# Kernel tuning notes

Measured on AMD Instinct MI355X. Metric: run time of the kernel, lower is better.

## Reference

```python
import jax, jax.numpy as jnp
import numpy as np

# dims: B batch, R seq_num (MSA rows), L seq_len (residues), D emb_dim, C n_emb_2D, H heads
B, R, L, D, C, H = 1, 256, 384, 512, 256, 4
HD = D // H
SCALE = np.float32((HD ** -0.5) / np.sqrt(L))  # head-dim scaling * seqlen_scaling (1/sqrt(L))
EPS = 1e-5


def setup_inputs() -> dict:
    key = jax.random.key(0)
    ks = jax.random.split(key, 6)
    s = 0.02
    return {
        "x": jax.random.normal(ks[0], (B, R, L, D), jnp.float32),
        "pair_feat": jax.random.normal(ks[1], (B, L, L, C), jnp.float32),
        "attn_mask": jnp.ones((B, L), jnp.int32),
        "ln_msa_g": jnp.ones((D,), jnp.float32),
        "ln_msa_b": jnp.zeros((D,), jnp.float32),
        "ln_pair_g": jnp.ones((C,), jnp.float32),
        "ln_pair_b": jnp.zeros((C,), jnp.float32),
        "W_pair": jax.random.normal(ks[2], (C, H), jnp.float32) * s,  # stacked per-head [C,1] linears
        "W_v": jax.random.normal(ks[3], (D, D), jnp.float32) * s,     # stacked per-head [D,HD] value proj
        "W_out": jax.random.normal(ks[4], (D, D), jnp.float32) * s,   # to_out (bias=False)
    }


def _ln(x, g, b):
    mu = jnp.mean(x, axis=-1, keepdims=True)
    var = jnp.mean(jnp.square(x - mu), axis=-1, keepdims=True)
    return (x - mu) * jax.lax.rsqrt(var + EPS) * g + b


def reference(x, pair_feat, attn_mask, ln_msa_g, ln_msa_b, ln_pair_g, ln_pair_b, W_pair, W_v, W_out):
    # MHPair_to_MSA.forward (eval mode, dropout=0)
    msa = _ln(x, ln_msa_g, ln_msa_b)                                  # [B,R,L,D]
    pf = (pair_feat + jnp.swapaxes(pair_feat, 1, 2)) * 0.5            # symmetrize
    pf = _ln(pf, ln_pair_g, ln_pair_b)                                # [B,L,L,C]
    # pair-feature-derived attention logits (no QK^T)
    logits = jnp.einsum('bijc,ch->bhij', pf * SCALE, W_pair)          # [B,H,L,L]
    V = jnp.einsum('brld,de->brle', msa, W_v).reshape(B, R, L, H, HD) # [B,R,L,H,HD]
    mask2 = attn_mask[:, :, None] * attn_mask[:, None, :]             # [B,L,L]
    logits = jnp.where(mask2[:, None, :, :] == 0,
                       jnp.finfo(logits.dtype).min, logits)
    attn = jax.nn.softmax(logits, axis=-1)                            # [B,H,L,L]
    out = jnp.einsum('bhij,brjhd->brihd', attn, V).reshape(B, R, L, D)
    out = out @ W_out                                                 # to_out, bias=False
    return x + out                                                    # residual
```

## Files before the change

### kernel.cpp

```cpp
#include <hip/hip_runtime.h>

#define L_   384
#define D_   512
#define C_   256
#define H_   4
#define RR_  256
#define M1_  98304
#define LL2_ 147456
#define NPAIR_BLOCKS 18480
#define TILE_ELEMS (128 * 64)
#define TILE256_ELEMS (256 * 64)

typedef __bf16 bf16x8 __attribute__((ext_vector_type(8)));
typedef float f32x4 __attribute__((ext_vector_type(4)));

__device__ __forceinline__ unsigned short f2bf_bits(float f) {
  union { float f; unsigned u; } v; v.f = f;
  return (unsigned short)((v.u + 0x7fffu + ((v.u >> 16) & 1u)) >> 16);
}
__device__ __forceinline__ __bf16 f2bf(float f) {
  union { unsigned short s; __bf16 b; } o; o.s = f2bf_bits(f);
  return o.b;
}

__device__ __forceinline__ float wave_sum(float v) {
#pragma unroll
  for (int o = 32; o > 0; o >>= 1) v += __shfl_xor(v, o);
  return v;
}
__device__ __forceinline__ float wave_max(float v) {
#pragma unroll
  for (int o = 32; o > 0; o >>= 1) v = fmaxf(v, __shfl_xor(v, o));
  return v;
}

__global__ __launch_bounds__(256) void ln_msa_kernel(
    const float* __restrict__ x, const float* __restrict__ g,
    const float* __restrict__ b, __bf16* __restrict__ msa) {
  int row = blockIdx.x * 4 + (threadIdx.x >> 6);
  int lane = threadIdx.x & 63;
  const float4* xr = (const float4*)(x + (size_t)row * D_ + lane * 8);
  float4 v0 = xr[0], v1 = xr[1];
  float s1 = v0.x + v0.y + v0.z + v0.w + v1.x + v1.y + v1.z + v1.w;
  float s2 = v0.x * v0.x + v0.y * v0.y + v0.z * v0.z + v0.w * v0.w +
             v1.x * v1.x + v1.y * v1.y + v1.z * v1.z + v1.w * v1.w;
#pragma unroll
  for (int o = 32; o > 0; o >>= 1) {
    s1 += __shfl_xor(s1, o);
    s2 += __shfl_xor(s2, o);
  }
  float mu = s1 * (1.0f / D_);
  float var = s2 * (1.0f / D_) - mu * mu;
  float rs = rsqrtf(var + 1e-5f);
  const float4* gp = (const float4*)(g + lane * 8);
  const float4* bp = (const float4*)(b + lane * 8);
  float4 g0 = gp[0], g1 = gp[1], b0 = bp[0], b1 = bp[1];
  float y[8];
  y[0] = (v0.x - mu) * rs * g0.x + b0.x;
  y[1] = (v0.y - mu) * rs * g0.y + b0.y;
  y[2] = (v0.z - mu) * rs * g0.z + b0.z;
  y[3] = (v0.w - mu) * rs * g0.w + b0.w;
  y[4] = (v1.x - mu) * rs * g1.x + b1.x;
  y[5] = (v1.y - mu) * rs * g1.y + b1.y;
  y[6] = (v1.z - mu) * rs * g1.z + b1.z;
  y[7] = (v1.w - mu) * rs * g1.w + b1.w;
  uint4 pk;
  pk.x = ((unsigned)f2bf_bits(y[1]) << 16) | f2bf_bits(y[0]);
  pk.y = ((unsigned)f2bf_bits(y[3]) << 16) | f2bf_bits(y[2]);
  pk.z = ((unsigned)f2bf_bits(y[5]) << 16) | f2bf_bits(y[4]);
  pk.w = ((unsigned)f2bf_bits(y[7]) << 16) | f2bf_bits(y[6]);
  *(uint4*)(msa + (size_t)row * D_ + lane * 8) = pk;
}

__global__ __launch_bounds__(256) void pair_logits_kernel(
    const float* __restrict__ pf, const int* __restrict__ mask,
    const float* __restrict__ g, const float* __restrict__ b,
    const float* __restrict__ Wp, float* __restrict__ logits) {
  unsigned wid = blockIdx.x * 4 + (threadIdx.x >> 6);
  int lane = threadIdx.x & 63;
  unsigned a = wid / 385u;
  unsigned c = wid - a * 385u;
  int i, j;
  if (c < 384u - a) { i = a; j = a + c; }
  else { i = 383 - a; j = i + (c - (384 - a)); }

  int c0 = lane * 4;
  float4 p1 = *(const float4*)(pf + ((size_t)i * L_ + j) * C_ + c0);
  float4 p2 = *(const float4*)(pf + ((size_t)j * L_ + i) * C_ + c0);
  float4 v;
  v.x = 0.5f * (p1.x + p2.x); v.y = 0.5f * (p1.y + p2.y);
  v.z = 0.5f * (p1.z + p2.z); v.w = 0.5f * (p1.w + p2.w);
  float s1 = v.x + v.y + v.z + v.w;
  float s2 = v.x * v.x + v.y * v.y + v.z * v.z + v.w * v.w;
#pragma unroll
  for (int o = 32; o > 0; o >>= 1) {
    s1 += __shfl_xor(s1, o);
    s2 += __shfl_xor(s2, o);
  }
  float mu = s1 * (1.0f / C_);
  float var = s2 * (1.0f / C_) - mu * mu;
  float rs = rsqrtf(var + 1e-5f);
  float4 gv = *(const float4*)(g + c0);
  float4 bv = *(const float4*)(b + c0);
  float y0 = (v.x - mu) * rs * gv.x + bv.x;
  float y1 = (v.y - mu) * rs * gv.y + bv.y;
  float y2 = (v.z - mu) * rs * gv.z + bv.z;
  float y3 = (v.w - mu) * rs * gv.w + bv.w;
  const float4* wp = (const float4*)Wp;
  float4 w0 = wp[c0], w1 = wp[c0 + 1], w2 = wp[c0 + 2], w3 = wp[c0 + 3];
  float4 t;
  t.x = y0 * w0.x + y1 * w1.x + y2 * w2.x + y3 * w3.x;
  t.y = y0 * w0.y + y1 * w1.y + y2 * w2.y + y3 * w3.y;
  t.z = y0 * w0.z + y1 * w1.z + y2 * w2.z + y3 * w3.z;
  t.w = y0 * w0.w + y1 * w1.w + y2 * w2.w + y3 * w3.w;
#pragma unroll
  for (int o = 32; o > 0; o >>= 1) {
    t.x += __shfl_xor(t.x, o);
    t.y += __shfl_xor(t.y, o);
    t.z += __shfl_xor(t.z, o);
    t.w += __shfl_xor(t.w, o);
  }
  if (lane < 8) {
    int h = lane & 3;
    int ii = (lane < 4) ? i : j;
    int jj = (lane < 4) ? j : i;
    bool ok = (mask[i] != 0) && (mask[j] != 0);
    const float NEG = -3.402823466e38f;
    const float SCALE = (float)(0.08838834764831845 / 19.595917942265423);
    float th = (h == 0) ? t.x : (h == 1) ? t.y : (h == 2) ? t.z : t.w;
    logits[(size_t)h * LL2_ + (size_t)ii * L_ + jj] = ok ? SCALE * th : NEG;
  }
}

__global__ __launch_bounds__(256) void softmax_kernel(
    const float* __restrict__ logits, __bf16* __restrict__ attn) {
  int wave = threadIdx.x >> 6, lane = threadIdx.x & 63;
  int row = blockIdx.x * 4 + wave;
  const float* lr = logits + (size_t)row * L_;
  float v[6];
#pragma unroll
  for (int t = 0; t < 6; ++t) v[t] = lr[lane + t * 64];
  float mx = v[0];
#pragma unroll
  for (int t = 1; t < 6; ++t) mx = fmaxf(mx, v[t]);
  mx = wave_max(mx);
  float s = 0.f;
#pragma unroll
  for (int t = 0; t < 6; ++t) { v[t] = __expf(v[t] - mx); s += v[t]; }
  s = wave_sum(s);
  float inv = 1.0f / s;
  __bf16* ar = attn + (size_t)row * L_;
#pragma unroll
  for (int t = 0; t < 6; ++t) ar[lane + t * 64] = f2bf(v[t] * inv);
}

__global__ __launch_bounds__(256) void wtrans_kernel(
    const float* __restrict__ Wv, const float* __restrict__ Wo,
    __bf16* __restrict__ WvT, __bf16* __restrict__ WoT) {
  int id = blockIdx.x * 256 + threadIdx.x;
  int m = id >> 18;
  int e = (id >> 9) & 511, d = id & 511;
  const float* W = m ? Wo : Wv;
  __bf16* T = m ? WoT : WvT;
  T[(size_t)e * 512 + d] = f2bf(W[(size_t)d * 512 + e]);
}

__device__ __forceinline__ void gload16(const void* g, void* l) {
  __builtin_amdgcn_global_load_lds(
      (const __attribute__((address_space(1))) void*)g,
      (__attribute__((address_space(3))) void*)l, 16, 0, 0);
}

__device__ __forceinline__ void stage_tile_async(__bf16* s, const __bf16* g, size_t ld) {
  int tid = threadIdx.x;
#pragma unroll
  for (int it = 0; it < 4; ++it) {
    int cid = it * 256 + tid;
    int row = cid >> 3, chk = cid & 7;
    int src_off = (chk * 16) ^ ((row & 7) << 4);
    gload16(g + (size_t)row * ld + (src_off >> 1), (char*)s + cid * 16);
  }
}

__device__ __forceinline__ void stage_tile256(__bf16* s, const __bf16* g, size_t ld) {
  int tid = threadIdx.x;
#pragma unroll
  for (int it = 0; it < 4; ++it) {
    int cid = it * 512 + tid;
    int row = cid >> 3, chk = cid & 7;
    int src_off = (chk * 16) ^ ((row & 7) << 4);
    gload16(g + (size_t)row * ld + (src_off >> 1), (char*)s + cid * 16);
  }
}

__device__ __forceinline__ bf16x8 frag_ld(const __bf16* s, int row, int k) {
  int sb = row * 128 + ((k * 2) ^ ((row & 7) << 4));
  return *(const bf16x8*)((const char*)s + sb);
}

__device__ __forceinline__ void gemm_mainloop(
    const __bf16* __restrict__ Arow, size_t ldA,
    const __bf16* __restrict__ Brow, size_t ldB,
    int K, __bf16* As, __bf16* Bs, f32x4 acc[4][4]) {
  int lane = threadIdx.x & 63, wave = threadIdx.x >> 6;
  int wm = (wave >> 1) * 64, wn = (wave & 1) * 64;
  int fr = lane & 15, fk = (lane >> 4) * 8;
  int nt = K >> 6;
  stage_tile_async(As, Arow, ldA);
  stage_tile_async(Bs, Brow, ldB);
  stage_tile_async(As + TILE_ELEMS, Arow + 64, ldA);
  stage_tile_async(Bs + TILE_ELEMS, Brow + 64, ldB);
  int cur = 0;
  for (int t = 0; t < nt; ++t) {
    if (t + 1 < nt) asm volatile("s_waitcnt vmcnt(8)" ::: "memory");
    else            asm volatile("s_waitcnt vmcnt(0)" ::: "memory");
    __builtin_amdgcn_s_barrier();
    __builtin_amdgcn_sched_barrier(0);
    const __bf16* Ab = As + cur * TILE_ELEMS;
    const __bf16* Bb = Bs + cur * TILE_ELEMS;
#pragma unroll
    for (int kk = 0; kk < 2; ++kk) {
      bf16x8 af[4], bfv[4];
#pragma unroll
      for (int mi = 0; mi < 4; ++mi) af[mi] = frag_ld(Ab, wm + mi * 16 + fr, kk * 32 + fk);
#pragma unroll
      for (int ni = 0; ni < 4; ++ni) bfv[ni] = frag_ld(Bb, wn + ni * 16 + fr, kk * 32 + fk);
#pragma unroll
      for (int mi = 0; mi < 4; ++mi)
#pragma unroll
        for (int ni = 0; ni < 4; ++ni)
          acc[mi][ni] = __builtin_amdgcn_mfma_f32_16x16x32_bf16(af[mi], bfv[ni], acc[mi][ni], 0, 0, 0);
    }
    __builtin_amdgcn_sched_barrier(0);
    __builtin_amdgcn_s_barrier();
    if (t + 2 < nt) {
      stage_tile_async(As + cur * TILE_ELEMS, Arow + (size_t)(t + 2) * 64, ldA);
      stage_tile_async(Bs + cur * TILE_ELEMS, Brow + (size_t)(t + 2) * 64, ldB);
    }
    cur ^= 1;
  }
}

__device__ __forceinline__ void gemm_mainloop256(
    const __bf16* __restrict__ Arow, size_t ldA,
    const __bf16* __restrict__ Brow, size_t ldB,
    int K, __bf16* As, __bf16* Bs, f32x4 acc[8][4]) {
  int lane = threadIdx.x & 63, wave = threadIdx.x >> 6;
  int wm = (wave >> 2) * 128, wn = (wave & 3) * 64;
  int fr = lane & 15, fk = (lane >> 4) * 8;
  int nt = K >> 6;
  stage_tile256(As, Arow, ldA);
  stage_tile256(Bs, Brow, ldB);
  stage_tile256(As + TILE256_ELEMS, Arow + 64, ldA);
  stage_tile256(Bs + TILE256_ELEMS, Brow + 64, ldB);
  int cur = 0;
  for (int t = 0; t < nt; ++t) {
    if (t + 1 < nt) asm volatile("s_waitcnt vmcnt(8)" ::: "memory");
    else            asm volatile("s_waitcnt vmcnt(0)" ::: "memory");
    __builtin_amdgcn_s_barrier();
    __builtin_amdgcn_sched_barrier(0);
    const __bf16* Ab = As + cur * TILE256_ELEMS;
    const __bf16* Bb = Bs + cur * TILE256_ELEMS;
#pragma unroll
    for (int kk = 0; kk < 2; ++kk) {
      bf16x8 af[8], bfv[4];
#pragma unroll
      for (int mi = 0; mi < 8; ++mi) af[mi] = frag_ld(Ab, wm + mi * 16 + fr, kk * 32 + fk);
#pragma unroll
      for (int ni = 0; ni < 4; ++ni) bfv[ni] = frag_ld(Bb, wn + ni * 16 + fr, kk * 32 + fk);
      __builtin_amdgcn_s_setprio(1);
#pragma unroll
      for (int mi = 0; mi < 8; ++mi)
#pragma unroll
        for (int ni = 0; ni < 4; ++ni)
          acc[mi][ni] = __builtin_amdgcn_mfma_f32_16x16x32_bf16(af[mi], bfv[ni], acc[mi][ni], 0, 0, 0);
      __builtin_amdgcn_s_setprio(0);
    }
    __builtin_amdgcn_sched_barrier(0);
    __builtin_amdgcn_s_barrier();
    if (t + 2 < nt) {
      stage_tile256(As + cur * TILE256_ELEMS, Arow + (size_t)(t + 2) * 64, ldA);
      stage_tile256(Bs + cur * TILE256_ELEMS, Brow + (size_t)(t + 2) * 64, ldB);
    }
    cur ^= 1;
  }
}

__device__ __forceinline__ unsigned xcd_swz_3072(unsigned bid) {
  return (bid & 7u) * 384u + (bid >> 3);
}
__device__ __forceinline__ unsigned xcd_swz_768(unsigned bid) {
  return (bid & 7u) * 96u + (bid >> 3);
}

__global__ __launch_bounds__(512, 1) void gemm_vt_kernel(
    const __bf16* __restrict__ WvT, const __bf16* __restrict__ msa,
    __bf16* __restrict__ VT) {
  __shared__ __bf16 As[2 * TILE256_ELEMS], Bs[2 * TILE256_ELEMS];
  unsigned swz = xcd_swz_768(blockIdx.x + 2 * blockIdx.y);
  int m0 = (swz & 1) * 256;
  int n0 = (swz >> 1) * 256;
  f32x4 acc[8][4] = {};
  gemm_mainloop256(WvT + (size_t)m0 * D_, D_, msa + (size_t)n0 * D_, D_, D_, As, Bs, acc);
  int lane = threadIdx.x & 63, wave = threadIdx.x >> 6;
  int wm = (wave >> 2) * 128, wn = (wave & 3) * 64;
  int cr = (lane >> 4) * 4, cc = lane & 15;
#pragma unroll
  for (int mi = 0; mi < 8; ++mi)
#pragma unroll
    for (int ni = 0; ni < 4; ++ni)
#pragma unroll
      for (int rr = 0; rr < 4; ++rr) {
        int row = m0 + wm + mi * 16 + cr + rr;
        int col = n0 + wn + ni * 16 + cc;
        VT[(size_t)row * M1_ + col] = f2bf(acc[mi][ni][rr]);
      }
}

__global__ __launch_bounds__(256) void attnv_kernel(
    const __bf16* __restrict__ attn, const __bf16* __restrict__ VT,
    __bf16* __restrict__ out2) {
  __shared__ __bf16 As[2 * TILE_ELEMS], Bs[2 * TILE_ELEMS];
  unsigned swz = xcd_swz_3072(blockIdx.x + 3 * blockIdx.y);
  int it = swz % 3u;
  int rh = swz / 3u;
  int h = rh & 3, r = rh >> 2;
  const __bf16* A = attn + (size_t)h * LL2_ + (size_t)it * 128 * L_;
  const __bf16* Bt = VT + (size_t)(h * 128) * M1_ + (size_t)r * L_;
  f32x4 acc[4][4] = {};
  gemm_mainloop(A, L_, Bt, M1_, L_, As, Bs, acc);
  int lane = threadIdx.x & 63, wave = threadIdx.x >> 6;
  int wm = (wave >> 1) * 64, wn = (wave & 1) * 64;
  int cr = (lane >> 4) * 4, cc = lane & 15;
#pragma unroll
  for (int mi = 0; mi < 4; ++mi)
#pragma unroll
    for (int ni = 0; ni < 4; ++ni)
#pragma unroll
      for (int rr = 0; rr < 4; ++rr) {
        int row_i = it * 128 + wm + mi * 16 + cr + rr;
        int col = h * 128 + wn + ni * 16 + cc;
        out2[((size_t)r * L_ + row_i) * D_ + col] = f2bf(acc[mi][ni][rr]);
      }
}

__global__ __launch_bounds__(512, 1) void gemm_out_kernel(
    const __bf16* __restrict__ out2, const __bf16* __restrict__ WoT,
    const float* __restrict__ x, float* __restrict__ out) {
  __shared__ __bf16 As[2 * TILE256_ELEMS], Bs[2 * TILE256_ELEMS];
  unsigned swz = xcd_swz_768(blockIdx.x + 2 * blockIdx.y);
  int n0 = (swz & 1) * 256;
  int m0 = (swz >> 1) * 256;
  f32x4 acc[8][4] = {};
  gemm_mainloop256(out2 + (size_t)m0 * D_, D_, WoT + (size_t)n0 * D_, D_, D_, As, Bs, acc);
  int lane = threadIdx.x & 63, wave = threadIdx.x >> 6;
  int wm = (wave >> 2) * 128, wn = (wave & 3) * 64;
  int cr = (lane >> 4) * 4, cc = lane & 15;
#pragma unroll
  for (int mi = 0; mi < 8; ++mi)
#pragma unroll
    for (int ni = 0; ni < 4; ++ni)
#pragma unroll
      for (int rr = 0; rr < 4; ++rr) {
        int row = m0 + wm + mi * 16 + cr + rr;
        int col = n0 + wn + ni * 16 + cc;
        size_t idx = (size_t)row * D_ + col;
        out[idx] = x[idx] + acc[mi][ni][rr];
      }
}

extern "C" void kernel_launch(void* const* d_in, const int* in_sizes, int n_in,
                              void* d_out, int out_size, void* d_ws, size_t ws_size,
                              hipStream_t stream) {
  const float* x      = (const float*)d_in[0];
  const float* pair   = (const float*)d_in[1];
  const int*   mask   = (const int*)d_in[2];
  const float* g_msa  = (const float*)d_in[3];
  const float* b_msa  = (const float*)d_in[4];
  const float* g_pair = (const float*)d_in[5];
  const float* b_pair = (const float*)d_in[6];
  const float* Wp     = (const float*)d_in[7];
  const float* Wv     = (const float*)d_in[8];
  const float* Wo     = (const float*)d_in[9];
  float* out = (float*)d_out;

  char* p = (char*)d_ws;
  auto alloc = [&](size_t bytes) {
    char* r = p;
    p += (bytes + 255) & ~(size_t)255;
    return r;
  };
  __bf16* msa    = (__bf16*)alloc((size_t)M1_ * D_ * 2);
  __bf16* VT     = (__bf16*)alloc((size_t)D_ * M1_ * 2);
  float*  logits = (float*)alloc((size_t)H_ * LL2_ * 4);
  __bf16* attn   = (__bf16*)alloc((size_t)H_ * LL2_ * 2);
  __bf16* WvT    = (__bf16*)alloc((size_t)512 * 512 * 2);
  __bf16* WoT    = (__bf16*)alloc((size_t)512 * 512 * 2);
  __bf16* out2   = msa;

  wtrans_kernel<<<2048, 256, 0, stream>>>(Wv, Wo, WvT, WoT);
  ln_msa_kernel<<<M1_ / 4, 256, 0, stream>>>(x, g_msa, b_msa, msa);
  gemm_vt_kernel<<<dim3(2, M1_ / 256), 512, 0, stream>>>(WvT, msa, VT);
  pair_logits_kernel<<<NPAIR_BLOCKS, 256, 0, stream>>>(pair, mask, g_pair, b_pair, Wp, logits);
  softmax_kernel<<<(H_ * L_) / 4, 256, 0, stream>>>(logits, attn);
  attnv_kernel<<<dim3(3, RR_ * H_), 256, 0, stream>>>(attn, VT, out2);
  gemm_out_kernel<<<dim3(2, M1_ / 256), 512, 0, stream>>>(out2, WoT, x, out);
}
```

Baseline: 375.7 us.

## Switch GEMM mainloops to 4-slot BK=32 ring buffer with single barrier

Replaces the double-buffered BK=64 pipelines in all three GEMM kernels with a four-slot ring of BK=32 stages that prefetches three tiles ahead. Each iteration now uses one barrier instead of two, and the next stage is issued before the MFMA work. The LDS swizzle is changed to fit 64-byte rows. The intent is to hide global load latency better and cut synchronisation. In exchange there are twice as many iterations and barriers per K, and the waitcnt accounting for the deeper pipeline is more delicate.

Result: no change. 376.3 us (+0.2%).

```diff
diff --git a/kernel.cpp b/kernel.cpp
--- a/kernel.cpp
+++ b/kernel.cpp
@@ -8,8 +8,6 @@
 #define M1_  98304
 #define LL2_ 147456
 #define NPAIR_BLOCKS 18480
-#define TILE_ELEMS (128 * 64)
-#define TILE256_ELEMS (256 * 64)
 
 typedef __bf16 bf16x8 __attribute__((ext_vector_type(8)));
 typedef float f32x4 __attribute__((ext_vector_type(4)));
@@ -171,118 +169,117 @@
       (__attribute__((address_space(3))) void*)l, 16, 0, 0);
 }
 
-__device__ __forceinline__ void stage_tile_async(__bf16* s, const __bf16* g, size_t ld) {
+template <int NT>
+__device__ __forceinline__ void stage_part32(__bf16* s, const __bf16* g, size_t ld) {
   int tid = threadIdx.x;
 #pragma unroll
-  for (int it = 0; it < 4; ++it) {
-    int cid = it * 256 + tid;
-    int row = cid >> 3, chk = cid & 7;
-    int src_off = (chk * 16) ^ ((row & 7) << 4);
-    gload16(g + (size_t)row * ld + (src_off >> 1), (char*)s + cid * 16);
-  }
-}
-
-__device__ __forceinline__ void stage_tile256(__bf16* s, const __bf16* g, size_t ld) {
-  int tid = threadIdx.x;
-#pragma unroll
-  for (int it = 0; it < 4; ++it) {
-    int cid = it * 512 + tid;
-    int row = cid >> 3, chk = cid & 7;
-    int src_off = (chk * 16) ^ ((row & 7) << 4);
-    gload16(g + (size_t)row * ld + (src_off >> 1), (char*)s + cid * 16);
-  }
-}
-
-__device__ __forceinline__ bf16x8 frag_ld(const __bf16* s, int row, int k) {
-  int sb = row * 128 + ((k * 2) ^ ((row & 7) << 4));
-  return *(const bf16x8*)((const char*)s + sb);
-}
-
-__device__ __forceinline__ void gemm_mainloop(
-    const __bf16* __restrict__ Arow, size_t ldA,
-    const __bf16* __restrict__ Brow, size_t ldB,
-    int K, __bf16* As, __bf16* Bs, f32x4 acc[4][4]) {
+  for (int i = 0; i < 2; ++i) {
+    int cid = i * NT + tid;
+    int row = cid >> 2, c = cid & 3;
+    int cs = c ^ ((row >> 1) & 3);
+    gload16(g + (size_t)row * ld + cs * 8, (char*)s + cid * 16);
+  }
+}
+
+__device__ __forceinline__ bf16x8 frag_ld32(const __bf16* s, int row, int fk) {
+  int c = (fk >> 3) ^ ((row >> 1) & 3);
+  return *(const bf16x8*)((const char*)s + row * 64 + c * 16);
+}
+
+
+__device__ __forceinline__ void mainloop256(
+    const __bf16* __restrict__ A, size_t ldA,
+    const __bf16* __restrict__ B, size_t ldB,
+    int K, __bf16* lds, f32x4 acc[8][4]) {
+  int lane = threadIdx.x & 63, wave = threadIdx.x >> 6;
+  int wm = (wave >> 2) * 128, wn = (wave & 3) * 64;
+  int fr = lane & 15, fk = (lane >> 4) * 8;
+  int nt = K >> 5;
+  const int SLOT = 512 * 32;
+#pragma unroll
+  for (int t = 0; t < 3; ++t) {
+    stage_part32<512>(lds + t * SLOT, A + t * 32, ldA);
+    stage_part32<512>(lds + t * SLOT + 256 * 32, B + t * 32, ldB);
+  }
+  for (int t = 0; t < nt; ++t) {
+    int rem = nt - 1 - t;
+    if (rem >= 2)      asm volatile("s_waitcnt vmcnt(8)" ::: "memory");
+    else if (rem == 1) asm volatile("s_waitcnt vmcnt(4)" ::: "memory");
+    else               asm volatile("s_waitcnt vmcnt(0)" ::: "memory");
+    __builtin_amdgcn_s_barrier();
+    const __bf16* As = lds + (t & 3) * SLOT;
+    const __bf16* Bs = As + 256 * 32;
+    if (t + 3 < nt) {
+      __bf16* d = lds + ((t + 3) & 3) * SLOT;
+      stage_part32<512>(d, A + (size_t)(t + 3) * 32, ldA);
+      stage_part32<512>(d + 256 * 32, B + (size_t)(t + 3) * 32, ldB);
+    }
+    bf16x8 bfv[4];
+#pragma unroll
+    for (int ni = 0; ni < 4; ++ni) bfv[ni] = frag_ld32(Bs, wn + ni * 16 + fr, fk);
+#pragma unroll
+    for (int half = 0; half < 2; ++half) {
+      bf16x8 af[4];
+#pragma unroll
+      for (int mi = 0; mi < 4; ++mi)
+        af[mi] = frag_ld32(As, wm + half * 64 + mi * 16 + fr, fk);
+      __builtin_amdgcn_s_setprio(1);
+#pragma unroll
+      for (int mi = 0; mi < 4; ++mi)
+#pragma unroll
+        for (int ni = 0; ni < 4; ++ni)
+          acc[half * 4 + mi][ni] = __builtin_amdgcn_mfma_f32_16x16x32_bf16(
+              af[mi], bfv[ni], acc[half * 4 + mi][ni], 0, 0, 0);
+      __builtin_amdgcn_s_setprio(0);
+    }
+  }
+}
+
+__device__ __forceinline__ void mainloop128(
+    const __bf16* __restrict__ A, size_t ldA,
+    const __bf16* __restrict__ B, size_t ldB,
+    int K, __bf16* lds, f32x4 acc[4][4]) {
   int lane = threadIdx.x & 63, wave = threadIdx.x >> 6;
   int wm = (wave >> 1) * 64, wn = (wave & 1) * 64;
   int fr = lane & 15, fk = (lane >> 4) * 8;
-  int nt = K >> 6;
-  stage_tile_async(As, Arow, ldA);
-  stage_tile_async(Bs, Brow, ldB);
-  stage_tile_async(As + TILE_ELEMS, Arow + 64, ldA);
-  stage_tile_async(Bs + TILE_ELEMS, Brow + 64, ldB);
-  int cur = 0;
+  int nt = K >> 5;
+  const int SLOT = 256 * 32;
+#pragma unroll
+  for (int t = 0; t < 3; ++t) {
+    stage_part32<256>(lds + t * SLOT, A + t * 32, ldA);
+    stage_part32<256>(lds + t * SLOT + 128 * 32, B + t * 32, ldB);
+  }
   for (int t = 0; t < nt; ++t) {
-    if (t + 1 < nt) asm volatile("s_waitcnt vmcnt(8)" ::: "memory");
-    else            asm volatile("s_waitcnt vmcnt(0)" ::: "memory");
+    int rem = nt - 1 - t;
+    if (rem >= 2)      asm volatile("s_waitcnt vmcnt(8)" ::: "memory");
+    else if (rem == 1) asm volatile("s_waitcnt vmcnt(4)" ::: "memory");
+    else               asm volatile("s_waitcnt vmcnt(0)" ::: "memory");
     __builtin_amdgcn_s_barrier();
-    __builtin_amdgcn_sched_barrier(0);
-    const __bf16* Ab = As + cur * TILE_ELEMS;
-    const __bf16* Bb = Bs + cur * TILE_ELEMS;
-#pragma unroll
-    for (int kk = 0; kk < 2; ++kk) {
-      bf16x8 af[4], bfv[4];
-#pragma unroll
-      for (int mi = 0; mi < 4; ++mi) af[mi] = frag_ld(Ab, wm + mi * 16 + fr, kk * 32 + fk);
-#pragma unroll
-      for (int ni = 0; ni < 4; ++ni) bfv[ni] = frag_ld(Bb, wn + ni * 16 + fr, kk * 32 + fk);
-#pragma unroll
-      for (int mi = 0; mi < 4; ++mi)
+    const __bf16* As = lds + (t & 3) * SLOT;
+    const __bf16* Bs = As + 128 * 32;
+    if (t + 3 < nt) {
+      __bf16* d = lds + ((t + 3) & 3) * SLOT;
+      stage_part32<256>(d, A + (size_t)(t + 3) * 32, ldA);
+      stage_part32<256>(d + 128 * 32, B + (size_t)(t + 3) * 32, ldB);
+    }
+    bf16x8 bfv[4];
+#pragma unroll
+    for (int ni = 0; ni < 4; ++ni) bfv[ni] = frag_ld32(Bs, wn + ni * 16 + fr, fk);
+#pragma unroll
+    for (int half = 0; half < 2; ++half) {
+      bf16x8 af[2];
+#pragma unroll
+      for (int mi = 0; mi < 2; ++mi)
+        af[mi] = frag_ld32(As, wm + half * 32 + mi * 16 + fr, fk);
+      __builtin_amdgcn_s_setprio(1);
+#pragma unroll
+      for (int mi = 0; mi < 2; ++mi)
 #pragma unroll
         for (int ni = 0; ni < 4; ++ni)
-          acc[mi][ni] = __builtin_amdgcn_mfma_f32_16x16x32_bf16(af[mi], bfv[ni], acc[mi][ni], 0, 0, 0);
-    }
-    __builtin_amdgcn_sched_barrier(0);
-    __builtin_amdgcn_s_barrier();
-    if (t + 2 < nt) {
-      stage_tile_async(As + cur * TILE_ELEMS, Arow + (size_t)(t + 2) * 64, ldA);
-      stage_tile_async(Bs + cur * TILE_ELEMS, Brow + (size_t)(t + 2) * 64, ldB);
-    }
-    cur ^= 1;
-  }
-}
-
-__device__ __forceinline__ void gemm_mainloop256(
-    const __bf16* __restrict__ Arow, size_t ldA,
-    const __bf16* __restrict__ Brow, size_t ldB,
-    int K, __bf16* As, __bf16* Bs, f32x4 acc[8][4]) {
-  int lane = threadIdx.x & 63, wave = threadIdx.x >> 6;
-  int wm = (wave >> 2) * 128, wn = (wave & 3) * 64;
-  int fr = lane & 15, fk = (lane >> 4) * 8;
-  int nt = K >> 6;
-  stage_tile256(As, Arow, ldA);
-  stage_tile256(Bs, Brow, ldB);
-  stage_tile256(As + TILE256_ELEMS, Arow + 64, ldA);
-  stage_tile256(Bs + TILE256_ELEMS, Brow + 64, ldB);
-  int cur = 0;
-  for (int t = 0; t < nt; ++t) {
-    if (t + 1 < nt) asm volatile("s_waitcnt vmcnt(8)" ::: "memory");
-    else            asm volatile("s_waitcnt vmcnt(0)" ::: "memory");
-    __builtin_amdgcn_s_barrier();
-    __builtin_amdgcn_sched_barrier(0);
-    const __bf16* Ab = As + cur * TILE256_ELEMS;
-    const __bf16* Bb = Bs + cur * TILE256_ELEMS;
-#pragma unroll
-    for (int kk = 0; kk < 2; ++kk) {
-      bf16x8 af[8], bfv[4];
-#pragma unroll
-      for (int mi = 0; mi < 8; ++mi) af[mi] = frag_ld(Ab, wm + mi * 16 + fr, kk * 32 + fk);
-#pragma unroll
-      for (int ni = 0; ni < 4; ++ni) bfv[ni] = frag_ld(Bb, wn + ni * 16 + fr, kk * 32 + fk);
-      __builtin_amdgcn_s_setprio(1);
-#pragma unroll
-      for (int mi = 0; mi < 8; ++mi)
-#pragma unroll
-        for (int ni = 0; ni < 4; ++ni)
-          acc[mi][ni] = __builtin_amdgcn_mfma_f32_16x16x32_bf16(af[mi], bfv[ni], acc[mi][ni], 0, 0, 0);
+          acc[half * 2 + mi][ni] = __builtin_amdgcn_mfma_f32_16x16x32_bf16(
+              af[mi], bfv[ni], acc[half * 2 + mi][ni], 0, 0, 0);
       __builtin_amdgcn_s_setprio(0);
     }
-    __builtin_amdgcn_sched_barrier(0);
-    __builtin_amdgcn_s_barrier();
-    if (t + 2 < nt) {
-      stage_tile256(As + cur * TILE256_ELEMS, Arow + (size_t)(t + 2) * 64, ldA);
-      stage_tile256(Bs + cur * TILE256_ELEMS, Brow + (size_t)(t + 2) * 64, ldB);
-    }
-    cur ^= 1;
   }
 }
 
@@ -296,12 +293,12 @@
 __global__ __launch_bounds__(512, 1) void gemm_vt_kernel(
     const __bf16* __restrict__ WvT, const __bf16* __restrict__ msa,
     __bf16* __restrict__ VT) {
-  __shared__ __bf16 As[2 * TILE256_ELEMS], Bs[2 * TILE256_ELEMS];
+  __shared__ __bf16 lds[4 * 512 * 32];
   unsigned swz = xcd_swz_768(blockIdx.x + 2 * blockIdx.y);
   int m0 = (swz & 1) * 256;
   int n0 = (swz >> 1) * 256;
   f32x4 acc[8][4] = {};
-  gemm_mainloop256(WvT + (size_t)m0 * D_, D_, msa + (size_t)n0 * D_, D_, D_, As, Bs, acc);
+  mainloop256(WvT + (size_t)m0 * D_, D_, msa + (size_t)n0 * D_, D_, D_, lds, acc);
   int lane = threadIdx.x & 63, wave = threadIdx.x >> 6;
   int wm = (wave >> 2) * 128, wn = (wave & 3) * 64;
   int cr = (lane >> 4) * 4, cc = lane & 15;
@@ -320,7 +317,7 @@
 __global__ __launch_bounds__(256) void attnv_kernel(
     const __bf16* __restrict__ attn, const __bf16* __restrict__ VT,
     __bf16* __restrict__ out2) {
-  __shared__ __bf16 As[2 * TILE_ELEMS], Bs[2 * TILE_ELEMS];
+  __shared__ __bf16 lds[4 * 256 * 32];
   unsigned swz = xcd_swz_3072(blockIdx.x + 3 * blockIdx.y);
   int it = swz % 3u;
   int rh = swz / 3u;
@@ -328,7 +325,7 @@
   const __bf16* A = attn + (size_t)h * LL2_ + (size_t)it * 128 * L_;
   const __bf16* Bt = VT + (size_t)(h * 128) * M1_ + (size_t)r * L_;
   f32x4 acc[4][4] = {};
-  gemm_mainloop(A, L_, Bt, M1_, L_, As, Bs, acc);
+  mainloop128(A, L_, Bt, M1_, L_, lds, acc);
   int lane = threadIdx.x & 63, wave = threadIdx.x >> 6;
   int wm = (wave >> 1) * 64, wn = (wave & 1) * 64;
   int cr = (lane >> 4) * 4, cc = lane & 15;
@@ -347,12 +344,12 @@
 __global__ __launch_bounds__(512, 1) void gemm_out_kernel(
     const __bf16* __restrict__ out2, const __bf16* __restrict__ WoT,
     const float* __restrict__ x, float* __restrict__ out) {
-  __shared__ __bf16 As[2 * TILE256_ELEMS], Bs[2 * TILE256_ELEMS];
+  __shared__ __bf16 lds[4 * 512 * 32];
   unsigned swz = xcd_swz_768(blockIdx.x + 2 * blockIdx.y);
   int n0 = (swz & 1) * 256;
   int m0 = (swz >> 1) * 256;
   f32x4 acc[8][4] = {};
-  gemm_mainloop256(out2 + (size_t)m0 * D_, D_, WoT + (size_t)n0 * D_, D_, D_, As, Bs, acc);
+  mainloop256(out2 + (size_t)m0 * D_, D_, WoT + (size_t)n0 * D_, D_, D_, lds, acc);
   int lane = threadIdx.x & 63, wave = threadIdx.x >> 6;
   int wm = (wave >> 2) * 128, wn = (wave & 3) * 64;
   int cr = (lane >> 4) * 4, cc = lane & 15;
```
